# Performance work log

Hardware: AMD Instinct MI355X
Metric: run time of the kernel (lower is better)

The kernel has to match this reference:

```python
import jax, jax.numpy as jnp
import numpy as np

T = 1024      # tokens
H = 2048      # hidden_size
I = 1408      # moe_intermediate_size
E = 16        # n_routed_experts
K = 6         # num_experts_per_tok
SI = I * 2    # shared experts intermediate (n_shared_experts=2)


def setup_inputs() -> dict:
    key = jax.random.key(0)
    ks = jax.random.split(key, 8)
    s = 0.02
    return {
        "x": jax.random.normal(ks[0], (T, H), jnp.float32),
        "gate_w": jax.random.normal(ks[1], (E, H), jnp.float32) * s,
        "w_gate": jax.random.normal(ks[2], (E, I, H), jnp.float32) * s,
        "w_up": jax.random.normal(ks[3], (E, I, H), jnp.float32) * s,
        "w_down": jax.random.normal(ks[4], (E, H, I), jnp.float32) * s,
        "sw_gate": jax.random.normal(ks[5], (SI, H), jnp.float32) * s,
        "sw_up": jax.random.normal(ks[6], (SI, H), jnp.float32) * s,
        "sw_down": jax.random.normal(ks[7], (H, SI), jnp.float32) * s,
    }


def reference(x, gate_w, w_gate, w_up, w_down, sw_gate, sw_up, sw_down):
    t = x.shape[0]
    # ---- router: softmax over experts, top-k, renormalize (norm_topk_prob) ----
    logits = x @ gate_w.T                                   # [T, E]
    probs = jax.nn.softmax(logits.astype(jnp.float32), axis=-1)
    topw, topi = jax.lax.top_k(probs, K)                    # [T, K]
    topw = topw / jnp.sum(topw, axis=-1, keepdims=True)
    # per-token per-expert combine weight (0 for unselected experts)
    comb = jnp.zeros((t, E), probs.dtype).at[
        jnp.arange(t)[:, None], topi
    ].add(topw)                                             # [T, E]

    # ---- routed experts: SwiGLU MLP per expert, weighted combine ----
    g = jnp.einsum('th,eih->tei', x, w_gate)                # [T, E, I]
    u = jnp.einsum('th,eih->tei', x, w_up)                  # [T, E, I]
    h = jax.nn.silu(g) * u                                  # [T, E, I]
    routed = jnp.einsum('te,tei,ehi->th', comb, h, w_down)  # [T, H]

    # ---- shared experts (always-on SwiGLU MLP) ----
    shared = (jax.nn.silu(x @ sw_gate.T) * (x @ sw_up.T)) @ sw_down.T  # [T, H]

    return routed + shared
```

## Files before the change

### kernel.cpp

```cpp
#include <hip/hip_runtime.h>
#include <stdint.h>

#define T_TOK 1024
#define H_DIM 2048
#define I_DIM 1408
#define IPAD 1536
#define E_NUM 16
#define K_TOP 6
#define PADCAP 8192
#define NE_ALL 18

typedef __attribute__((ext_vector_type(8))) short short8;
typedef __attribute__((ext_vector_type(8))) unsigned short ushort8;
typedef __attribute__((ext_vector_type(4))) float f32x4;

__device__ __forceinline__ unsigned short f2b(float f) {
    unsigned u = __float_as_uint(f);
    u += 0x7fffu + ((u >> 16) & 1u);
    return (unsigned short)(u >> 16);
}
__device__ __forceinline__ float b2f(unsigned short s) {
    return __uint_as_float((unsigned)s << 16);
}

__device__ __forceinline__ unsigned cvt_pk2(float a, float b) {
    unsigned r;
    asm("v_cvt_pk_bf16_f32 %0, %1, %2" : "=v"(r) : "v"(a), "v"(b));
    return r;
}

typedef __attribute__((address_space(1))) const unsigned int as1_uint;
typedef __attribute__((address_space(3))) unsigned int as3_uint;
__device__ __forceinline__ void gload16(const void* g, void* l) {
    __builtin_amdgcn_global_load_lds((as1_uint*)g, (as3_uint*)l, 16, 0, 0);
}

#define SCHED0() __builtin_amdgcn_sched_barrier(0)

__device__ __forceinline__ int xcd_swizzle(int bid, int nwg) {
    const int q = nwg >> 3, r = nwg & 7;
    const int xcd = bid & 7, k = bid >> 3;
    const int base = (xcd < r) ? xcd * (q + 1) : r * (q + 1) + (xcd - r) * q;
    return base + k;
}

__global__ __launch_bounds__(256) void router_kernel(
    const float* __restrict__ x, const float* __restrict__ gw,
    float* __restrict__ topw, int* __restrict__ eidx, int* __restrict__ slotarr,
    int* __restrict__ counts)
{
    const int t = blockIdx.x, tid = threadIdx.x;
    const int lane = tid & 63, wave = tid >> 6;
    float part[E_NUM];
#pragma unroll
    for (int e = 0; e < E_NUM; ++e) part[e] = 0.f;
    const float* xr = x + (size_t)t * H_DIM;
    for (int i = tid; i < H_DIM; i += 256) {
        float xv = xr[i];
#pragma unroll
        for (int e = 0; e < E_NUM; ++e) part[e] += xv * gw[e * H_DIM + i];
    }
    __shared__ float red[4][E_NUM];
#pragma unroll
    for (int e = 0; e < E_NUM; ++e) {
        float v = part[e];
        for (int off = 32; off; off >>= 1) v += __shfl_down(v, off);
        if (lane == 0) red[wave][e] = v;
    }
    __syncthreads();
    if (tid == 0) {
        float logits[E_NUM];
#pragma unroll
        for (int e = 0; e < E_NUM; ++e)
            logits[e] = red[0][e] + red[1][e] + red[2][e] + red[3][e];
        int sel[K_TOP]; float selv[K_TOP];
        unsigned used = 0;
        for (int k = 0; k < K_TOP; ++k) {
            int best = 0; float bv = -1e30f;
            for (int e = 0; e < E_NUM; ++e)
                if (!((used >> e) & 1u) && logits[e] > bv) { bv = logits[e]; best = e; }
            used |= 1u << best; sel[k] = best; selv[k] = bv;
        }
        float mx = selv[0], s = 0.f, w[K_TOP];
        for (int k = 0; k < K_TOP; ++k) { w[k] = expf(selv[k] - mx); s += w[k]; }
        float inv = 1.f / s;
        for (int k = 0; k < K_TOP; ++k) {
            int slot = atomicAdd(&counts[sel[k]], 1);
            topw[t * K_TOP + k] = w[k] * inv;
            eidx[t * K_TOP + k] = sel[k];
            slotarr[t * K_TOP + k] = slot;
        }
    }
}

__global__ void zero_counts_kernel(int* counts) {
    if (threadIdx.x < E_NUM) counts[threadIdx.x] = 0;
}

__global__ void prefix_kernel(const int* __restrict__ counts, int* __restrict__ offs) {
    if (threadIdx.x == 0) {
        int o = 0;
        for (int e = 0; e < E_NUM; ++e) { offs[e] = o; o += (counts[e] + 127) & ~127; }
        offs[E_NUM] = o;
    }
}

__global__ __launch_bounds__(256) void gather_cvt_kernel(
    const float* __restrict__ x, const int* __restrict__ eidx,
    const int* __restrict__ slotarr, const int* __restrict__ offs,
    ushort* __restrict__ Xall)
{
    const int b = blockIdx.x;
    int t; size_t row;
    if (b < T_TOK * K_TOP) {
        t = b / K_TOP;
        row = (size_t)offs[eidx[b]] + (size_t)slotarr[b];
    } else {
        t = b - T_TOK * K_TOP;
        row = (size_t)offs[E_NUM] + (size_t)t;
    }
    const float* src = x + (size_t)t * H_DIM;
    ushort* dst = Xall + row * H_DIM;
    const int i = threadIdx.x * 8;
    float4 f0 = *(const float4*)(src + i);
    float4 f1 = *(const float4*)(src + i + 4);
    ushort8 v;
    v[0] = f2b(f0.x); v[1] = f2b(f0.y); v[2] = f2b(f0.z); v[3] = f2b(f0.w);
    v[4] = f2b(f1.x); v[5] = f2b(f1.y); v[6] = f2b(f1.z); v[7] = f2b(f1.w);
    *(ushort8*)(dst + i) = v;
}

template<int DOWN>
__global__ __launch_bounds__(512, 2) void moe_gemm_kernel(
    const ushort* __restrict__ Abase,
    const float* __restrict__ Wr1, const float* __restrict__ Wr2,
    const float* __restrict__ Ws1, const float* __restrict__ Ws2,
    ushort* __restrict__ C1, ushort* __restrict__ C2,
    const int* __restrict__ counts, const int* __restrict__ offs,
    int nNT, int lda, int K, int ldc)
{
    __shared__ short Alds[2][128 * 64];
    __shared__ short Blds[2][256 * 64];

    const int work = xcd_swizzle(blockIdx.x, gridDim.x);
    const int slab = NE_ALL * 8;
    int nt = work / slab;
    const int rem = work - nt * slab;
    const int e = rem >> 3;
    const int mt = rem & 7;

    const int S = offs[E_NUM];
    const int M = (e < E_NUM) ? counts[e] : 1024;
    const int row0 = mt << 7;
    if (row0 >= M) return;
    const int crowbase = (e < E_NUM) ? offs[e] : S + ((e - E_NUM) << 10);
    const int arowbase = DOWN ? crowbase : ((e < E_NUM) ? offs[e] : S);

    const float* B; ushort* C; int ldb, koff = 0, NB;
    if (DOWN) {
        NB = H_DIM; C = C1;
        if (e < E_NUM) { ldb = I_DIM; B = Wr1 + (size_t)e * H_DIM * I_DIM; }
        else           { ldb = 2 * I_DIM; B = Ws1; koff = (e - E_NUM) * I_DIM; }
    } else {
        NB = I_DIM; ldb = H_DIM;
        const float* Bg = (e < E_NUM) ? Wr1 + (size_t)e * I_DIM * H_DIM
                                      : Ws1 + (size_t)(e - E_NUM) * I_DIM * H_DIM;
        const float* Bu = (e < E_NUM) ? Wr2 + (size_t)e * I_DIM * H_DIM
                                      : Ws2 + (size_t)(e - E_NUM) * I_DIM * H_DIM;
        if (nt < nNT) { B = Bg; C = C1; } else { B = Bu; C = C2; nt -= nNT; }
    }
    const int n0 = nt << 8;

    const int tid = threadIdx.x;
    const int lane = tid & 63;
    const int wave = tid >> 6;
    const int wm = wave >> 2, wn = wave & 3;
    const int l15 = lane & 15, lhi = lane >> 4;

    const char* __restrict__ Ab = (const char*)(Abase + (size_t)(arowbase + row0) * lda);

    int aOff[2];
#pragma unroll
    for (int i = 0; i < 2; ++i) {
        const int chunk = wave * 2 + i;
        const int off = chunk * 1024 + lane * 16;
        const int r = off >> 7, s = (off >> 4) & 7;
        aOff[i] = r * lda * 2 + ((s ^ (r & 7)) << 4);
    }

    const int brow = tid >> 3, bsl = tid & 7;
    const float* Bc[4]; int bldw[4];
#pragma unroll
    for (int j = 0; j < 4; ++j) {
        const int rl = brow + (j << 6);
        const int rg = min(n0 + rl, NB - 1);
        Bc[j] = B + (size_t)rg * ldb + koff + (bsl << 3);
        bldw[j] = (rl << 6) + ((bsl ^ (rl & 7)) << 3);
    }

    f32x4 acc[4][4];
#pragma unroll
    for (int m = 0; m < 4; ++m)
#pragma unroll
        for (int n = 0; n < 4; ++n) acc[m][n] = (f32x4){0.f, 0.f, 0.f, 0.f};

    float4 br[4][2];

    auto issueA = [&](int kt, int pb) {
#pragma unroll
        for (int i = 0; i < 2; ++i)
            gload16(Ab + (size_t)aOff[i] + (size_t)(kt << 7),
                    (char*)Alds[pb] + (wave * 2 + i) * 1024);
    };
    auto issueB = [&](int kt) {
#pragma unroll
        for (int j = 0; j < 4; ++j) {
            const float* src = Bc[j] + (kt << 6);
            br[j][0] = *(const float4*)src;
            br[j][1] = *(const float4*)(src + 4);
        }
    };
    auto writeB = [&](int pb) {
#pragma unroll
        for (int j = 0; j < 4; ++j) {
            union { short8 s; unsigned u[4]; } w;
            w.u[0] = cvt_pk2(br[j][0].x, br[j][0].y);
            w.u[1] = cvt_pk2(br[j][0].z, br[j][0].w);
            w.u[2] = cvt_pk2(br[j][1].x, br[j][1].y);
            w.u[3] = cvt_pk2(br[j][1].z, br[j][1].w);
            *(short8*)&Blds[pb][bldw[j]] = w.s;
        }
    };
    auto compute = [&](int p) {
#pragma unroll
        for (int kk = 0; kk < 2; ++kk) {
            const int kb = (kk << 2) + lhi;
            short8 af[4], bfr[4];
#pragma unroll
            for (int m = 0; m < 4; ++m) {
                const int rA = (wm << 6) + (m << 4) + l15;
                af[m] = *(const short8*)&Alds[p][(rA << 6) + ((kb ^ (rA & 7)) << 3)];
            }
#pragma unroll
            for (int n = 0; n < 4; ++n) {
                const int rB = (wn << 6) + (n << 4) + l15;
                bfr[n] = *(const short8*)&Blds[p][(rB << 6) + ((kb ^ (rB & 7)) << 3)];
            }
            __builtin_amdgcn_s_setprio(1);
#pragma unroll
            for (int m = 0; m < 4; ++m)
#pragma unroll
                for (int n = 0; n < 4; ++n)
                    acc[m][n] = __builtin_amdgcn_mfma_f32_16x16x32_bf16(
                        af[m], bfr[n], acc[m][n], 0, 0, 0);
            __builtin_amdgcn_s_setprio(0);
        }
    };

    const int nK = K >> 6;
    issueA(0, 0); SCHED0();
    issueB(0); SCHED0();
    writeB(0);
    __syncthreads();

    int p = 0;
    for (int kt = 0; kt < nK; ++kt) {
        const bool more = (kt + 1 < nK);
        if (more) {
            issueA(kt + 1, p ^ 1); SCHED0();
            issueB(kt + 1); SCHED0();
        }
        compute(p);
        if (more) writeB(p ^ 1);
        __syncthreads();
        p ^= 1;
    }

    const size_t cbase_col = (size_t)n0 + (wn << 6) + l15;
#pragma unroll
    for (int m = 0; m < 4; ++m) {
        const int rloc = (wm << 6) + (m << 4) + (lhi << 2);
#pragma unroll
        for (int j = 0; j < 4; ++j) {
            const int crow = row0 + rloc + j;
            if (crow >= M) continue;
            const size_t co = (size_t)(crowbase + crow) * ldc + cbase_col;
#pragma unroll
            for (int n = 0; n < 4; ++n) C[co + (n << 4)] = f2b(acc[m][n][j]);
        }
    }
}

__global__ __launch_bounds__(256) void silu_kernel(
    ushort* __restrict__ G, const ushort* __restrict__ U,
    const int* __restrict__ eidx, const int* __restrict__ slotarr,
    const int* __restrict__ offs)
{
    const int b = blockIdx.x;
    size_t row;
    if (b < T_TOK * K_TOP) {
        row = (size_t)offs[eidx[b]] + (size_t)slotarr[b];
    } else {
        row = (size_t)offs[E_NUM] + (size_t)(b - T_TOK * K_TOP);
    }
    ushort* g = G + row * IPAD;
    const ushort* u = U + row * IPAD;
    const int i = threadIdx.x * 8;
    if (i < I_DIM) {
        ushort8 gv = *(const ushort8*)(g + i);
        ushort8 uv = *(const ushort8*)(u + i);
        ushort8 hv;
#pragma unroll
        for (int j = 0; j < 8; ++j) {
            float gf = b2f(gv[j]);
            float uf = b2f(uv[j]);
            float sf = gf / (1.f + expf(-gf));
            hv[j] = f2b(sf * uf);
        }
        *(ushort8*)(g + i) = hv;
    }
}

__global__ __launch_bounds__(256) void combine_kernel(
    float* __restrict__ out, const ushort* __restrict__ Y,
    const float* __restrict__ topw, const int* __restrict__ eidx,
    const int* __restrict__ slotarr, const int* __restrict__ offs)
{
    const int t = blockIdx.x;
    const int i = threadIdx.x * 8;
    const int S = offs[E_NUM];
    float acc[8];
    {
        ushort8 v0 = *(const ushort8*)(Y + ((size_t)S + t) * H_DIM + i);
        ushort8 v1 = *(const ushort8*)(Y + ((size_t)S + 1024 + t) * H_DIM + i);
#pragma unroll
        for (int j = 0; j < 8; ++j) acc[j] = b2f(v0[j]) + b2f(v1[j]);
    }
#pragma unroll
    for (int k = 0; k < K_TOP; ++k) {
        const float w = topw[t * K_TOP + k];
        const size_t row = (size_t)offs[eidx[t * K_TOP + k]] + (size_t)slotarr[t * K_TOP + k];
        ushort8 v = *(const ushort8*)(Y + row * H_DIM + i);
#pragma unroll
        for (int j = 0; j < 8; ++j) acc[j] += w * b2f(v[j]);
    }
    float* o = out + (size_t)t * H_DIM;
    float4 o0, o1;
    o0.x = acc[0]; o0.y = acc[1]; o0.z = acc[2]; o0.w = acc[3];
    o1.x = acc[4]; o1.y = acc[5]; o1.z = acc[6]; o1.w = acc[7];
    *(float4*)(o + i) = o0;
    *(float4*)(o + i + 4) = o1;
}

extern "C" void kernel_launch(void* const* d_in, const int* in_sizes, int n_in,
                              void* d_out, int out_size, void* d_ws, size_t ws_size,
                              hipStream_t stream) {
    const float* x       = (const float*)d_in[0];
    const float* gate_w  = (const float*)d_in[1];
    const float* w_gate  = (const float*)d_in[2];
    const float* w_up    = (const float*)d_in[3];
    const float* w_down  = (const float*)d_in[4];
    const float* sw_gate = (const float*)d_in[5];
    const float* sw_up   = (const float*)d_in[6];
    const float* sw_down = (const float*)d_in[7];
    float* out = (float*)d_out;

    char* p = (char*)d_ws;
    auto take = [&](size_t b) { char* r = p; p += (b + 255) & ~(size_t)255; return r; };
    int*    counts = (int*)take(32 * 4);
    int*    offs   = (int*)take(32 * 4);
    float*  topw   = (float*)take((size_t)T_TOK * K_TOP * 4);
    int*    eidx   = (int*)take((size_t)T_TOK * K_TOP * 4);
    int*    slot   = (int*)take((size_t)T_TOK * K_TOP * 4);
    ushort* Xall   = (ushort*)take((size_t)(PADCAP + 1024) * H_DIM * 2);
    ushort* G      = (ushort*)take((size_t)(PADCAP + 2048) * IPAD * 2);
    ushort* U      = (ushort*)take((size_t)(PADCAP + 2048) * IPAD * 2);
    ushort* Y      = (ushort*)take((size_t)(PADCAP + 2048) * H_DIM * 2);

    zero_counts_kernel<<<1, 64, 0, stream>>>(counts);
    router_kernel<<<T_TOK, 256, 0, stream>>>(x, gate_w, topw, eidx, slot, counts);
    prefix_kernel<<<1, 64, 0, stream>>>(counts, offs);
    gather_cvt_kernel<<<T_TOK * K_TOP + T_TOK, 256, 0, stream>>>(x, eidx, slot, offs, Xall);

    moe_gemm_kernel<0><<<12 * NE_ALL * 8, 512, 0, stream>>>(
        Xall, w_gate, w_up, sw_gate, sw_up, G, U, counts, offs,
        6, H_DIM , H_DIM , IPAD );
    silu_kernel<<<T_TOK * K_TOP + 2048, 256, 0, stream>>>(G, U, eidx, slot, offs);
    moe_gemm_kernel<1><<<8 * NE_ALL * 8, 512, 0, stream>>>(
        G, w_down, nullptr, sw_down, nullptr, Y, nullptr, counts, offs,
        8, IPAD , I_DIM , H_DIM );

    combine_kernel<<<T_TOK, 256, 0, stream>>>(out, Y, topw, eidx, slot, offs);
}
```

Baseline: 564.0 us.

## Shrink MoE GEMM tile to 128x128 with 256 threads and single-buffered B

Changes the grouped GEMM from 512-thread 128x256 tiles to 256-thread 128x128 tiles, which doubles the number of N tiles and removes the IPAD padding (1408 divides exactly by 128). The B LDS buffer becomes single-buffered, guarded by explicit barriers and waitcnt, so LDS use drops and three workgroups can fit per CU. The aim is better occupancy, and avoiding wasted work on padded columns. The cost is that A tiles are reloaded twice as often across N tiles, and the extra barrier per k-step may serialize the B write against compute.

```diff
diff --git a/kernel.cpp b/kernel.cpp
--- a/kernel.cpp
+++ b/kernel.cpp
@@ -4,7 +4,6 @@
 #define T_TOK 1024
 #define H_DIM 2048
 #define I_DIM 1408
-#define IPAD 1536
 #define E_NUM 16
 #define K_TOP 6
 #define PADCAP 8192
@@ -36,6 +35,7 @@
 }
 
 #define SCHED0() __builtin_amdgcn_sched_barrier(0)
+#define RBAR() __builtin_amdgcn_s_barrier()
 
 __device__ __forceinline__ int xcd_swizzle(int bid, int nwg) {
     const int q = nwg >> 3, r = nwg & 7;
@@ -131,7 +131,7 @@
 }
 
 template<int DOWN>
-__global__ __launch_bounds__(512, 2) void moe_gemm_kernel(
+__global__ __launch_bounds__(256, 3) void moe_gemm_kernel(
     const ushort* __restrict__ Abase,
     const float* __restrict__ Wr1, const float* __restrict__ Wr2,
     const float* __restrict__ Ws1, const float* __restrict__ Ws2,
@@ -140,7 +140,7 @@
     int nNT, int lda, int K, int ldc)
 {
     __shared__ short Alds[2][128 * 64];
-    __shared__ short Blds[2][256 * 64];
+    __shared__ short Blds[128 * 64];
 
     const int work = xcd_swizzle(blockIdx.x, gridDim.x);
     const int slab = NE_ALL * 8;
@@ -156,46 +156,45 @@
     const int crowbase = (e < E_NUM) ? offs[e] : S + ((e - E_NUM) << 10);
     const int arowbase = DOWN ? crowbase : ((e < E_NUM) ? offs[e] : S);
 
-    const float* B; ushort* C; int ldb, koff = 0, NB;
+    const float* B; ushort* C; int ldb, koff = 0;
     if (DOWN) {
-        NB = H_DIM; C = C1;
+        C = C1;
         if (e < E_NUM) { ldb = I_DIM; B = Wr1 + (size_t)e * H_DIM * I_DIM; }
         else           { ldb = 2 * I_DIM; B = Ws1; koff = (e - E_NUM) * I_DIM; }
     } else {
-        NB = I_DIM; ldb = H_DIM;
+        ldb = H_DIM;
         const float* Bg = (e < E_NUM) ? Wr1 + (size_t)e * I_DIM * H_DIM
                                       : Ws1 + (size_t)(e - E_NUM) * I_DIM * H_DIM;
         const float* Bu = (e < E_NUM) ? Wr2 + (size_t)e * I_DIM * H_DIM
                                       : Ws2 + (size_t)(e - E_NUM) * I_DIM * H_DIM;
         if (nt < nNT) { B = Bg; C = C1; } else { B = Bu; C = C2; nt -= nNT; }
     }
-    const int n0 = nt << 8;
+    const int n0 = nt << 7;
 
     const int tid = threadIdx.x;
     const int lane = tid & 63;
     const int wave = tid >> 6;
-    const int wm = wave >> 2, wn = wave & 3;
+    const int wm = wave & 1, wn = wave >> 1;
     const int l15 = lane & 15, lhi = lane >> 4;
 
     const char* __restrict__ Ab = (const char*)(Abase + (size_t)(arowbase + row0) * lda);
 
-    int aOff[2];
-#pragma unroll
-    for (int i = 0; i < 2; ++i) {
-        const int chunk = wave * 2 + i;
+    int aOff[4];
+#pragma unroll
+    for (int i = 0; i < 4; ++i) {
+        const int chunk = wave * 4 + i;
         const int off = chunk * 1024 + lane * 16;
         const int r = off >> 7, s = (off >> 4) & 7;
         aOff[i] = r * lda * 2 + ((s ^ (r & 7)) << 4);
     }
 
-    const int brow = tid >> 3, bsl = tid & 7;
+    const int br_ = tid >> 3, bs = tid & 7;
     const float* Bc[4]; int bldw[4];
 #pragma unroll
-    for (int j = 0; j < 4; ++j) {
-        const int rl = brow + (j << 6);
-        const int rg = min(n0 + rl, NB - 1);
-        Bc[j] = B + (size_t)rg * ldb + koff + (bsl << 3);
-        bldw[j] = (rl << 6) + ((bsl ^ (rl & 7)) << 3);
+    for (int i = 0; i < 4; ++i) {
+        const int r = br_ + (i << 5);
+        Bc[i] = B + (size_t)(n0 + r) * ldb + koff + (bs << 3);
+        bldw[i] = (r << 6) + ((bs ^ (r & 7)) << 3);
     }
 
     f32x4 acc[4][4];
@@ -206,29 +205,29 @@
 
     float4 br[4][2];
 
+    auto issueB = [&](int kt) {
+#pragma unroll
+        for (int i = 0; i < 4; ++i) {
+            const float* src = Bc[i] + (kt << 6);
+            br[i][0] = *(const float4*)src;
+            br[i][1] = *(const float4*)(src + 4);
+        }
+    };
     auto issueA = [&](int kt, int pb) {
 #pragma unroll
-        for (int i = 0; i < 2; ++i)
+        for (int i = 0; i < 4; ++i)
             gload16(Ab + (size_t)aOff[i] + (size_t)(kt << 7),
-                    (char*)Alds[pb] + (wave * 2 + i) * 1024);
+                    (char*)Alds[pb] + (wave * 4 + i) * 1024);
     };
-    auto issueB = [&](int kt) {
-#pragma unroll
-        for (int j = 0; j < 4; ++j) {
-            const float* src = Bc[j] + (kt << 6);
-            br[j][0] = *(const float4*)src;
-            br[j][1] = *(const float4*)(src + 4);
-        }
-    };
-    auto writeB = [&](int pb) {
-#pragma unroll
-        for (int j = 0; j < 4; ++j) {
+    auto writeB = [&]() {
+#pragma unroll
+        for (int i = 0; i < 4; ++i) {
             union { short8 s; unsigned u[4]; } w;
-            w.u[0] = cvt_pk2(br[j][0].x, br[j][0].y);
-            w.u[1] = cvt_pk2(br[j][0].z, br[j][0].w);
-            w.u[2] = cvt_pk2(br[j][1].x, br[j][1].y);
-            w.u[3] = cvt_pk2(br[j][1].z, br[j][1].w);
-            *(short8*)&Blds[pb][bldw[j]] = w.s;
+            w.u[0] = cvt_pk2(br[i][0].x, br[i][0].y);
+            w.u[1] = cvt_pk2(br[i][0].z, br[i][0].w);
+            w.u[2] = cvt_pk2(br[i][1].x, br[i][1].y);
+            w.u[3] = cvt_pk2(br[i][1].z, br[i][1].w);
+            *(short8*)&Blds[bldw[i]] = w.s;
         }
     };
     auto compute = [&](int p) {
@@ -244,7 +243,7 @@
 #pragma unroll
             for (int n = 0; n < 4; ++n) {
                 const int rB = (wn << 6) + (n << 4) + l15;
-                bfr[n] = *(const short8*)&Blds[p][(rB << 6) + ((kb ^ (rB & 7)) << 3)];
+                bfr[n] = *(const short8*)&Blds[(rB << 6) + ((kb ^ (rB & 7)) << 3)];
             }
             __builtin_amdgcn_s_setprio(1);
 #pragma unroll
@@ -258,22 +257,27 @@
     };
 
     const int nK = K >> 6;
+    issueB(0); SCHED0();
     issueA(0, 0); SCHED0();
-    issueB(0); SCHED0();
-    writeB(0);
-    __syncthreads();
+    writeB();
+    asm volatile("s_waitcnt vmcnt(0) lgkmcnt(0)" ::: "memory");
+    RBAR(); SCHED0();
 
     int p = 0;
     for (int kt = 0; kt < nK; ++kt) {
         const bool more = (kt + 1 < nK);
         if (more) {
+            issueB(kt + 1); SCHED0();
             issueA(kt + 1, p ^ 1); SCHED0();
-            issueB(kt + 1); SCHED0();
         }
         compute(p);
-        if (more) writeB(p ^ 1);
-        __syncthreads();
-        p ^= 1;
+        if (more) {
+            RBAR();
+            writeB();
+            asm volatile("s_waitcnt vmcnt(0) lgkmcnt(0)" ::: "memory");
+            RBAR(); SCHED0();
+            p ^= 1;
+        }
     }
 
     const size_t cbase_col = (size_t)n0 + (wn << 6) + l15;
@@ -303,8 +307,8 @@
     } else {
         row = (size_t)offs[E_NUM] + (size_t)(b - T_TOK * K_TOP);
     }
-    ushort* g = G + row * IPAD;
-    const ushort* u = U + row * IPAD;
+    ushort* g = G + row * I_DIM;
+    const ushort* u = U + row * I_DIM;
     const int i = threadIdx.x * 8;
     if (i < I_DIM) {
         ushort8 gv = *(const ushort8*)(g + i);
@@ -373,8 +377,8 @@
     int*    eidx   = (int*)take((size_t)T_TOK * K_TOP * 4);
     int*    slot   = (int*)take((size_t)T_TOK * K_TOP * 4);
     ushort* Xall   = (ushort*)take((size_t)(PADCAP + 1024) * H_DIM * 2);
-    ushort* G      = (ushort*)take((size_t)(PADCAP + 2048) * IPAD * 2);
-    ushort* U      = (ushort*)take((size_t)(PADCAP + 2048) * IPAD * 2);
+    ushort* G      = (ushort*)take((size_t)(PADCAP + 2048) * I_DIM * 2);
+    ushort* U      = (ushort*)take((size_t)(PADCAP + 2048) * I_DIM * 2);
     ushort* Y      = (ushort*)take((size_t)(PADCAP + 2048) * H_DIM * 2);
 
     zero_counts_kernel<<<1, 64, 0, stream>>>(counts);
@@ -382,13 +386,13 @@
     prefix_kernel<<<1, 64, 0, stream>>>(counts, offs);
     gather_cvt_kernel<<<T_TOK * K_TOP + T_TOK, 256, 0, stream>>>(x, eidx, slot, offs, Xall);
 
-    moe_gemm_kernel<0><<<12 * NE_ALL * 8, 512, 0, stream>>>(
+    moe_gemm_kernel<0><<<22 * NE_ALL * 8, 256, 0, stream>>>(
         Xall, w_gate, w_up, sw_gate, sw_up, G, U, counts, offs,
-        6, H_DIM , H_DIM , IPAD );
+        11, H_DIM , H_DIM , I_DIM );
     silu_kernel<<<T_TOK * K_TOP + 2048, 256, 0, stream>>>(G, U, eidx, slot, offs);
-    moe_gemm_kernel<1><<<8 * NE_ALL * 8, 512, 0, stream>>>(
+    moe_gemm_kernel<1><<<16 * NE_ALL * 8, 256, 0, stream>>>(
         G, w_down, nullptr, sw_down, nullptr, Y, nullptr, counts, offs,
-        8, IPAD , I_DIM , H_DIM );
+        16, I_DIM , I_DIM , H_DIM );
 
     combine_kernel<<<T_TOK, 256, 0, stream>>>(out, Y, topw, eidx, slot, offs);
 }
```

After: 468.1 us, median of 2. -17.0%, faster.
